# Kernel tuning notes

Hardware: AMD Instinct MI355X
Metric: run time of the kernel (lower is better)

Reference implementation:

```python
import jax, jax.numpy as jnp
import numpy as np

N, E, F, H, L, G = 100000, 1600000, 128, 128, 8, 256
EPS = 1e-5


def setup_inputs() -> dict:
    key = jax.random.key(0)
    ks = jax.random.split(key, 12)
    s = 0.05
    return {
        "x": jax.random.normal(ks[0], (N, F), jnp.float32),
        "edge_index": jax.random.randint(ks[1], (2, E), 0, N, dtype=jnp.int32),
        "batch": jnp.sort(jax.random.randint(ks[2], (N,), 0, G, dtype=jnp.int32)),
        # input projection
        "Wp": jax.random.normal(ks[3], (F, H), jnp.float32) * s,
        "bp": jnp.zeros((H,), jnp.float32),
        # stacked residual-block params (L blocks, 2 GCNConv+BN each)
        "W1": jax.random.normal(ks[4], (L, H, H), jnp.float32) * s,
        "b1": jnp.zeros((L, H), jnp.float32),
        "g1": jnp.ones((L, H), jnp.float32),
        "be1": jnp.zeros((L, H), jnp.float32),
        "W2": jax.random.normal(ks[5], (L, H, H), jnp.float32) * s,
        "b2": jnp.zeros((L, H), jnp.float32),
        "g2": jnp.ones((L, H), jnp.float32),
        "be2": jnp.zeros((L, H), jnp.float32),
        # readout MLP: 3H -> 2H -> H -> 1
        "Wa": jax.random.normal(ks[6], (3 * H, 2 * H), jnp.float32) * s,
        "ba": jnp.zeros((2 * H,), jnp.float32),
        "Wb": jax.random.normal(ks[7], (2 * H, H), jnp.float32) * s,
        "bb": jnp.zeros((H,), jnp.float32),
        "Wc": jax.random.normal(ks[8], (H, 1), jnp.float32) * s,
        "bc": jnp.zeros((1,), jnp.float32),
    }


def _bn(h, g, b):
    # BatchNorm over the node dimension (training-style batch stats, eps=1e-5)
    mu = h.mean(0)
    var = h.var(0)
    return (h - mu) * jax.lax.rsqrt(var + EPS) * g + b


def reference(x, edge_index, batch, Wp, bp, W1, b1, g1, be1, W2, b2, g2, be2,
              Wa, ba, Wb, bb, Wc, bc):
    src, dst = edge_index[0], edge_index[1]
    # GCN symmetric norm with self-loops: deg = in-degree + 1
    deg = jnp.zeros((N,), x.dtype).at[dst].add(1.0) + 1.0
    dinv = jax.lax.rsqrt(deg)
    norm_e = (dinv[src] * dinv[dst])[:, None]   # [E,1]
    self_norm = (dinv * dinv)[:, None]          # [N,1]

    def gcn(h, W, b):
        hw = h @ W                                              # [N,H]
        agg = jnp.zeros_like(hw).at[dst].add(norm_e * hw[src])  # scatter-add over edges
        return agg + self_norm * hw + b                         # self-loop + bias

    h = x @ Wp + bp

    def step(h, p):
        w1, bb1, gg1, bbe1, w2, bb2, gg2, bbe2 = p
        o = jax.nn.relu(_bn(gcn(h, w1, bb1), gg1, bbe1))
        o = _bn(gcn(o, w2, bb2), gg2, bbe2)
        return h + o, None

    h, _ = jax.lax.scan(step, h, (W1, b1, g1, be1, W2, b2, g2, be2))

    sums = jax.ops.segment_sum(h, batch, num_segments=G)
    cnt = jax.ops.segment_sum(jnp.ones((N, 1), h.dtype), batch, num_segments=G)
    mean = sums / jnp.maximum(cnt, 1.0)
    mx = jax.ops.segment_max(h, batch, num_segments=G)
    z = jnp.concatenate([mean, mx, sums], axis=1)  # [G, 3H]

    z = jax.nn.relu(z @ Wa + ba)
    z = jax.nn.relu(z @ Wb + bb)
    return z @ Wc + bc  # [G, 1]
```

## Files before the change

kernel.cpp:

```cpp
#include <hip/hip_runtime.h>
#include <hip/hip_fp16.h>
#include <math.h>
#include <float.h>

#define HDIM 128
#define NGRAPH 256
#define EPSBN 1e-5f
#define PS_REP 32
#define SLABF (2 * PS_REP * 128)

typedef _Float16 f16x8 __attribute__((ext_vector_type(8)));
typedef _Float16 f16x4 __attribute__((ext_vector_type(4)));
typedef float f32x4 __attribute__((ext_vector_type(4)));

__device__ inline unsigned enc_f(float v) {
  unsigned u = __float_as_uint(v);
  return (u & 0x80000000u) ? ~u : (u | 0x80000000u);
}
__device__ inline float dec_f(unsigned e) {
  return __uint_as_float((e & 0x80000000u) ? (e ^ 0x80000000u) : ~e);
}

__global__ void k_deg(const int* __restrict__ dst, int* __restrict__ deg, int E) {
  int i = blockIdx.x * blockDim.x + threadIdx.x;
  if (i < E) atomicAdd(&deg[dst[i]], 1);
}

__global__ void k_dinv(const int* __restrict__ deg, float* __restrict__ dinv, int n) {
  int i = blockIdx.x * blockDim.x + threadIdx.x;
  if (i < n) dinv[i] = rsqrtf((float)deg[i] + 1.0f);
}

__global__ void k_scanA(const int* __restrict__ deg, int* __restrict__ rowstart,
                        int* __restrict__ bsum, int n) {
  __shared__ int s[256];
  int t = threadIdx.x, i = blockIdx.x * 256 + t;
  int v = (i < n) ? ((deg[i] + 3) & ~3) : 0;
  s[t] = v;
  __syncthreads();
  for (int off = 1; off < 256; off <<= 1) {
    int x = (t >= off) ? s[t - off] : 0;
    __syncthreads();
    s[t] += x;
    __syncthreads();
  }
  if (i < n) rowstart[i] = s[t] - v;
  if (t == 255) bsum[blockIdx.x] = s[255];
}

__global__ void k_scanB(int* __restrict__ bsum, int nb) {
  __shared__ int s[512];
  int t = threadIdx.x;
  int v = (t < nb) ? bsum[t] : 0;
  s[t] = v;
  __syncthreads();
  for (int off = 1; off < 512; off <<= 1) {
    int x = (t >= off) ? s[t - off] : 0;
    __syncthreads();
    s[t] += x;
    __syncthreads();
  }
  if (t < nb) bsum[t] = s[t] - v;
}

__global__ void k_scanC(int* __restrict__ rowstart, const int* __restrict__ bsum,
                        const int* __restrict__ deg, int n) {
  int i = blockIdx.x * 256 + threadIdx.x;
  if (i < n) {
    int v = rowstart[i] + bsum[blockIdx.x];
    rowstart[i] = v;
    if (i == n - 1) rowstart[n] = v + ((deg[i] + 3) & ~3);
  }
}

__global__ void k_fill(const int* __restrict__ src, const int* __restrict__ dst,
                       const float* __restrict__ dinv, const int* __restrict__ prow,
                       int* __restrict__ cursor, int2* __restrict__ csr2, int E) {
  int e = blockIdx.x * blockDim.x + threadIdx.x;
  if (e < E) {
    int d = dst[e], s = src[e];
    int pos = prow[d] + atomicAdd(&cursor[d], 1);
    csr2[pos] = make_int2(s << 8, __float_as_int(dinv[s] * dinv[d]));
  }
}

__global__ void k_pad(const int* __restrict__ deg, const int* __restrict__ prow,
                      int2* __restrict__ csr2, int n) {
  int i = blockIdx.x * blockDim.x + threadIdx.x;
  if (i < n) {
    int d = deg[i], dp = (d + 3) & ~3;
    int base = prow[i];
    for (int j = d; j < dp; ++j) csr2[base + j] = make_int2(i << 8, 0);
  }
}

__global__ __launch_bounds__(256) void k_wprep(const float* __restrict__ W1,
                                               const float* __restrict__ W2,
                                               const float* __restrict__ Wp,
                                               _Float16* __restrict__ wt) {
  int m = blockIdx.x;
  const float* Wsrc = (m == 16) ? Wp : (((m & 1) ? W2 : W1) + (size_t)(m >> 1) * 16384);
  _Float16* Wdst = wt + (size_t)m * 16384;
  __shared__ _Float16 lds[128 * 132];
  int t = threadIdx.x;
  const float4* W4 = (const float4*)Wsrc;
  for (int it = 0; it < 16; ++it) {
    int idx = t + it * 256;
    int k = idx >> 5, c4 = idx & 31;
    float4 v = W4[idx];
    lds[(c4 * 4 + 0) * 132 + k] = (_Float16)v.x;
    lds[(c4 * 4 + 1) * 132 + k] = (_Float16)v.y;
    lds[(c4 * 4 + 2) * 132 + k] = (_Float16)v.z;
    lds[(c4 * 4 + 3) * 132 + k] = (_Float16)v.w;
  }
  __syncthreads();
  for (int it = 0; it < 16; ++it) {
    int idx = t + it * 256;
    int col = idx >> 5, k4 = idx & 31;
    f16x4 o;
    o[0] = lds[col * 132 + k4 * 4 + 0];
    o[1] = lds[col * 132 + k4 * 4 + 1];
    o[2] = lds[col * 132 + k4 * 4 + 2];
    o[3] = lds[col * 132 + k4 * 4 + 3];
    *(f16x4*)(Wdst + col * 128 + k4 * 4) = o;
  }
}

__global__ __launch_bounds__(256) void k_gemmp(const float* __restrict__ in,
                                               const _Float16* __restrict__ wt,
                                               const float* __restrict__ bias,
                                               float* __restrict__ out, int n) {
  __shared__ _Float16 As[64 * 128];
  __shared__ _Float16 Bs[128 * 128];
  char* Ap = (char*)As;
  char* Bp = (char*)Bs;
  int tid = threadIdx.x;
  int lane = tid & 63;
  int rt = tid >> 6;
  int row0 = blockIdx.x * 64;

  for (int it = 0; it < 8; ++it) {
    int idx = tid + it * 256;
    int r = idx >> 5, c4 = idx & 31;
    int row = row0 + r;
    if (row >= n) row = n - 1;
    float4 v = *(const float4*)(in + (size_t)row * 128 + c4 * 4);
    f16x4 hv;
    hv[0] = (_Float16)v.x; hv[1] = (_Float16)v.y;
    hv[2] = (_Float16)v.z; hv[3] = (_Float16)v.w;
    *(f16x4*)(Ap + ((r * 256 + c4 * 8) ^ ((r & 7) << 4))) = hv;
  }
  for (int it = 0; it < 8; ++it) {
    int idx = tid + it * 256;
    int col = idx >> 4, k8 = idx & 15;
    f16x8 v = *(const f16x8*)(wt + col * 128 + k8 * 8);
    *(f16x8*)(Bp + ((col * 256 + k8 * 16) ^ ((col & 7) << 4))) = v;
  }
  __syncthreads();

  f32x4 acc[8];
#pragma unroll
  for (int ct = 0; ct < 8; ++ct) acc[ct] = (f32x4){0.f, 0.f, 0.f, 0.f};
  int arow = rt * 16 + (lane & 15);
  int kc = (lane >> 4) * 16;
#pragma unroll
  for (int ks = 0; ks < 4; ++ks) {
    int kb = ks * 64;
    f16x8 a = *(f16x8*)(Ap + ((arow * 256 + kb + kc) ^ ((arow & 7) << 4)));
#pragma unroll
    for (int ct = 0; ct < 8; ++ct) {
      int bcol = ct * 16 + (lane & 15);
      f16x8 b = *(f16x8*)(Bp + ((bcol * 256 + kb + kc) ^ ((bcol & 7) << 4)));
      acc[ct] = __builtin_amdgcn_mfma_f32_16x16x32_f16(a, b, acc[ct], 0, 0, 0);
    }
  }

  int orow0 = row0 + rt * 16 + (lane >> 4) * 4;
#pragma unroll
  for (int ct = 0; ct < 8; ++ct) {
    int col = ct * 16 + (lane & 15);
    float bb = bias[col];
#pragma unroll
    for (int r = 0; r < 4; ++r) {
      int row = orow0 + r;
      if (row < n) out[(size_t)row * 128 + col] = acc[ct][r] + bb;
    }
  }
}

template <int XFORM>
__global__ __launch_bounds__(256) void k_gemmh(const void* __restrict__ inp,
                                               const _Float16* __restrict__ wt,
                                               const float* __restrict__ psumL,
                                               const float* __restrict__ gg,
                                               const float* __restrict__ be,
                                               float* __restrict__ hres,
                                               _Float16* __restrict__ outh, int n) {
  __shared__ _Float16 As[64 * 128];
  __shared__ _Float16 Bs[128 * 128];
  __shared__ float sc_s[128], sh_s[128];
  char* Ap = (char*)As;
  char* Bp = (char*)Bs;
  int tid = threadIdx.x;
  int lane = tid & 63;
  int rt = tid >> 6;
  int row0 = blockIdx.x * 64;

  if (XFORM) {
    if (tid < 128) {
      const float* psqL = psumL + PS_REP * 128;
      float s = 0.f, q = 0.f;
#pragma unroll 8
      for (int r = 0; r < PS_REP; ++r) {
        s += psumL[r * 128 + tid];
        q += psqL[r * 128 + tid];
      }
      float mu = s / (float)n;
      float var = q / (float)n - mu * mu;
      float rs = rsqrtf(var + EPSBN);
      float sc = gg[tid] * rs;
      sc_s[tid] = sc;
      sh_s[tid] = be[tid] - mu * sc;
    }
    __syncthreads();
  }

  if (XFORM == 0) {
    const float* in = (const float*)inp;
    for (int it = 0; it < 8; ++it) {
      int idx = tid + it * 256;
      int r = idx >> 5, c4 = idx & 31;
      int row = row0 + r;
      if (row >= n) row = n - 1;
      float4 v = *(const float4*)(in + (size_t)row * 128 + c4 * 4);
      f16x4 hv16;
      hv16[0] = (_Float16)v.x; hv16[1] = (_Float16)v.y;
      hv16[2] = (_Float16)v.z; hv16[3] = (_Float16)v.w;
      *(f16x4*)(Ap + ((r * 256 + c4 * 8) ^ ((r & 7) << 4))) = hv16;
    }
  } else {
    const _Float16* in = (const _Float16*)inp;
    for (int it = 0; it < 4; ++it) {
      int idx = tid + it * 256;
      int r = idx >> 4, c8 = idx & 15;
      int rrow = row0 + r;
      int row = (rrow >= n) ? (n - 1) : rrow;
      f16x8 tv = *(const f16x8*)(in + (size_t)row * 128 + c8 * 8);
      float4 s0 = *(const float4*)(sc_s + c8 * 8);
      float4 s1 = *(const float4*)(sc_s + c8 * 8 + 4);
      float4 h0 = *(const float4*)(sh_s + c8 * 8);
      float4 h1 = *(const float4*)(sh_s + c8 * 8 + 4);
      float v[8];
#pragma unroll
      for (int j = 0; j < 8; ++j) v[j] = (float)tv[j];
      v[0] = v[0] * s0.x + h0.x; v[1] = v[1] * s0.y + h0.y;
      v[2] = v[2] * s0.z + h0.z; v[3] = v[3] * s0.w + h0.w;
      v[4] = v[4] * s1.x + h1.x; v[5] = v[5] * s1.y + h1.y;
      v[6] = v[6] * s1.z + h1.z; v[7] = v[7] * s1.w + h1.w;
      if (XFORM == 1) {
#pragma unroll
        for (int j = 0; j < 8; ++j) v[j] = fmaxf(v[j], 0.f);
      }
      if (XFORM == 2) {
        float4 hv0 = *(const float4*)(hres + (size_t)row * 128 + c8 * 8);
        float4 hv1 = *(const float4*)(hres + (size_t)row * 128 + c8 * 8 + 4);
        v[0] += hv0.x; v[1] += hv0.y; v[2] += hv0.z; v[3] += hv0.w;
        v[4] += hv1.x; v[5] += hv1.y; v[6] += hv1.z; v[7] += hv1.w;
        if (rrow < n) {
          *(float4*)(hres + (size_t)row * 128 + c8 * 8) = make_float4(v[0], v[1], v[2], v[3]);
          *(float4*)(hres + (size_t)row * 128 + c8 * 8 + 4) = make_float4(v[4], v[5], v[6], v[7]);
        }
      }
      f16x8 o;
#pragma unroll
      for (int j = 0; j < 8; ++j) o[j] = (_Float16)v[j];
      *(f16x8*)(Ap + ((r * 256 + c8 * 16) ^ ((r & 7) << 4))) = o;
    }
  }
  for (int it = 0; it < 8; ++it) {
    int idx = tid + it * 256;
    int col = idx >> 4, k8 = idx & 15;
    f16x8 v = *(const f16x8*)(wt + col * 128 + k8 * 8);
    *(f16x8*)(Bp + ((col * 256 + k8 * 16) ^ ((col & 7) << 4))) = v;
  }
  __syncthreads();

  f32x4 acc[8];
#pragma unroll
  for (int ct = 0; ct < 8; ++ct) acc[ct] = (f32x4){0.f, 0.f, 0.f, 0.f};

  int arow = rt * 16 + (lane & 15);
  int kc = (lane >> 4) * 16;
#pragma unroll
  for (int ks = 0; ks < 4; ++ks) {
    int kb = ks * 64;
    f16x8 a = *(f16x8*)(Ap + ((arow * 256 + kb + kc) ^ ((arow & 7) << 4)));
#pragma unroll
    for (int ct = 0; ct < 8; ++ct) {
      int bcol = ct * 16 + (lane & 15);
      f16x8 b = *(f16x8*)(Bp + ((bcol * 256 + kb + kc) ^ ((bcol & 7) << 4)));
      acc[ct] = __builtin_amdgcn_mfma_f32_16x16x32_f16(a, b, acc[ct], 0, 0, 0);
    }
  }

  int orow0 = row0 + rt * 16 + (lane >> 4) * 4;
#pragma unroll
  for (int ct = 0; ct < 8; ++ct) {
    int col = ct * 16 + (lane & 15);
#pragma unroll
    for (int r = 0; r < 4; ++r) {
      int row = orow0 + r;
      if (row < n) outh[(size_t)row * 128 + col] = (_Float16)acc[ct][r];
    }
  }
}

__global__ __launch_bounds__(256) void k_agg(const _Float16* __restrict__ hw,
                                             const int* __restrict__ prow,
                                             const int2* __restrict__ csr2,
                                             const float* __restrict__ dinv,
                                             const float* __restrict__ bias,
                                             _Float16* __restrict__ out,
                                             float* __restrict__ psumL, int n) {
  int wave = threadIdx.x >> 6;
  int lane = threadIdx.x & 63;
  int grp = lane >> 4;
  int l16 = lane & 15;
  int node = blockIdx.x * 4 + wave;
  float a[8];
#pragma unroll
  for (int j = 0; j < 8; ++j) a[j] = 0.f;

  if (node < n) {
    float b8[8];
#pragma unroll
    for (int j = 0; j < 8; ++j) b8[j] = 0.f;
    int e0 = prow[node], e1 = prow[node + 1];
    int len = e1 - e0;
    int e = e0;
    int end8 = e0 + (len & ~7);
    const char* base = (const char*)hw + l16 * 16;
    for (; e < end8; e += 8) {
      int4 pq = *(const int4*)(csr2 + e + 2 * grp);
      float w0 = __int_as_float(pq.y);
      float w1 = __int_as_float(pq.w);
      f16x8 v0 = *(const f16x8*)(base + (unsigned)pq.x);
      f16x8 v1 = *(const f16x8*)(base + (unsigned)pq.z);
#pragma unroll
      for (int j = 0; j < 8; ++j) {
        a[j] += w0 * (float)v0[j];
        b8[j] += w1 * (float)v1[j];
      }
    }
    if (len & 4) {
      int2 p = csr2[e + grp];
      float w = __int_as_float(p.y);
      f16x8 v = *(const f16x8*)(base + (unsigned)p.x);
#pragma unroll
      for (int j = 0; j < 8; ++j) a[j] += w * (float)v[j];
    }
#pragma unroll
    for (int j = 0; j < 8; ++j) a[j] += b8[j];
#pragma unroll
    for (int j = 0; j < 8; ++j) {
      a[j] += __shfl_xor(a[j], 16);
      a[j] += __shfl_xor(a[j], 32);
    }
    float dn = dinv[node];
    float sn = dn * dn;
    f16x8 v = *(const f16x8*)(hw + (size_t)node * 128 + l16 * 8);
    float4 bb0 = *(const float4*)(bias + l16 * 8);
    float4 bb1 = *(const float4*)(bias + l16 * 8 + 4);
    a[0] += sn * (float)v[0] + bb0.x;
    a[1] += sn * (float)v[1] + bb0.y;
    a[2] += sn * (float)v[2] + bb0.z;
    a[3] += sn * (float)v[3] + bb0.w;
    a[4] += sn * (float)v[4] + bb1.x;
    a[5] += sn * (float)v[5] + bb1.y;
    a[6] += sn * (float)v[6] + bb1.z;
    a[7] += sn * (float)v[7] + bb1.w;
    if (grp == 0) {
      f16x8 ov;
#pragma unroll
      for (int j = 0; j < 8; ++j) ov[j] = (_Float16)a[j];
      *(f16x8*)(out + (size_t)node * 128 + l16 * 8) = ov;
    }
  }
  __shared__ float ss[4][128];
  __shared__ float sq[4][128];
  if (grp == 0) {
    bool live = (node < n);
    float v0 = live ? a[0] : 0.f, v1 = live ? a[1] : 0.f;
    float v2 = live ? a[2] : 0.f, v3 = live ? a[3] : 0.f;
    float v4 = live ? a[4] : 0.f, v5 = live ? a[5] : 0.f;
    float v6 = live ? a[6] : 0.f, v7 = live ? a[7] : 0.f;
    *(float4*)&ss[wave][l16 * 8] = make_float4(v0, v1, v2, v3);
    *(float4*)&ss[wave][l16 * 8 + 4] = make_float4(v4, v5, v6, v7);
    *(float4*)&sq[wave][l16 * 8] = make_float4(v0 * v0, v1 * v1, v2 * v2, v3 * v3);
    *(float4*)&sq[wave][l16 * 8 + 4] = make_float4(v4 * v4, v5 * v5, v6 * v6, v7 * v7);
  }
  __syncthreads();
  int t = threadIdx.x;
  if (t < 128) {
    float s = (ss[0][t] + ss[1][t]) + (ss[2][t] + ss[3][t]);
    float q = (sq[0][t] + sq[1][t]) + (sq[2][t] + sq[3][t]);
    int rep = blockIdx.x & (PS_REP - 1);
    atomicAdd(&psumL[rep * 128 + t], s);
    atomicAdd(&psumL[PS_REP * 128 + rep * 128 + t], q);
  }
}

#define PCHUNK 128
__global__ __launch_bounds__(128) void k_pool(const float* __restrict__ h,
                                              const _Float16* __restrict__ t2h,
                                              const float* __restrict__ psumL,
                                              const float* __restrict__ gg,
                                              const float* __restrict__ be,
                                              const int* __restrict__ batch,
                                              float* __restrict__ sums,
                                              unsigned* __restrict__ maxenc,
                                              int* __restrict__ cnt, int n) {
  int c = threadIdx.x;
  __shared__ float sc_s[128], sh_s[128];
  {
    const float* psqL = psumL + PS_REP * 128;
    float s = 0.f, q = 0.f;
#pragma unroll 8
    for (int r = 0; r < PS_REP; ++r) {
      s += psumL[r * 128 + c];
      q += psqL[r * 128 + c];
    }
    float mu = s / (float)n;
    float var = q / (float)n - mu * mu;
    float rs = rsqrtf(var + EPSBN);
    float sc = gg[c] * rs;
    sc_s[c] = sc;
    sh_s[c] = be[c] - mu * sc;
  }
  __syncthreads();
  float scc = sc_s[c], shc = sh_s[c];

  int start = blockIdx.x * PCHUNK;
  if (start >= n) return;
  int end = start + PCHUNK;
  if (end > n) end = n;
  int cur = batch[start];
  float s = 0.f, mx = -FLT_MAX;
  int runlen = 0;
  for (int i = start; i < end; ++i) {
    int b = batch[i];
    if (b != cur) {
      atomicAdd(&sums[cur * 128 + c], s);
      atomicMax(&maxenc[cur * 128 + c], enc_f(mx));
      if (c == 0) atomicAdd(&cnt[cur], runlen);
      s = 0.f; mx = -FLT_MAX; runlen = 0; cur = b;
    }
    float v = h[(size_t)i * 128 + c] + scc * (float)t2h[(size_t)i * 128 + c] + shc;
    s += v;
    mx = fmaxf(mx, v);
    runlen++;
  }
  atomicAdd(&sums[cur * 128 + c], s);
  atomicMax(&maxenc[cur * 128 + c], enc_f(mx));
  if (c == 0) atomicAdd(&cnt[cur], runlen);
}

__global__ __launch_bounds__(256) void k_readout(const float* __restrict__ sums,
                                                 const unsigned* __restrict__ maxenc,
                                                 const int* __restrict__ cnt,
                                                 const float* __restrict__ Wa,
                                                 const float* __restrict__ ba,
                                                 const float* __restrict__ Wb,
                                                 const float* __restrict__ bb,
                                                 const float* __restrict__ Wc,
                                                 const float* __restrict__ bc,
                                                 float* __restrict__ out) {
  int g = blockIdx.x;
  int t = threadIdx.x;
  __shared__ float z[384];
  __shared__ float za[256];
  __shared__ float zb[128];
  float c = (float)(cnt[g] > 1 ? cnt[g] : 1);
  if (t < 128) {
    float s = sums[g * 128 + t];
    z[t] = s / c;
    z[128 + t] = dec_f(maxenc[g * 128 + t]);
    z[256 + t] = s;
  }
  __syncthreads();
  float accA = ba[t];
  for (int k = 0; k < 384; k++) accA += z[k] * Wa[k * 256 + t];
  za[t] = fmaxf(accA, 0.f);
  __syncthreads();
  if (t < 128) {
    float accB = bb[t];
    for (int k = 0; k < 256; k++) accB += za[k] * Wb[k * 128 + t];
    zb[t] = fmaxf(accB, 0.f);
  }
  __syncthreads();
  if (t < 64) {
    float p = zb[t] * Wc[t] + zb[t + 64] * Wc[t + 64];
    for (int off = 32; off > 0; off >>= 1) p += __shfl_down(p, off);
    if (t == 0) out[g] = p + bc[0];
  }
}

extern "C" void kernel_launch(void* const* d_in, const int* in_sizes, int n_in,
                              void* d_out, int out_size, void* d_ws, size_t ws_size,
                              hipStream_t stream) {
  const float* x   = (const float*)d_in[0];
  const int* edge  = (const int*)d_in[1];
  const int* batch = (const int*)d_in[2];
  const float* Wp  = (const float*)d_in[3];
  const float* bp  = (const float*)d_in[4];
  const float* W1  = (const float*)d_in[5];
  const float* b1  = (const float*)d_in[6];
  const float* g1  = (const float*)d_in[7];
  const float* be1 = (const float*)d_in[8];
  const float* W2  = (const float*)d_in[9];
  const float* b2  = (const float*)d_in[10];
  const float* g2  = (const float*)d_in[11];
  const float* be2 = (const float*)d_in[12];
  const float* Wa  = (const float*)d_in[13];
  const float* ba  = (const float*)d_in[14];
  const float* Wb  = (const float*)d_in[15];
  const float* bbp = (const float*)d_in[16];
  const float* Wc  = (const float*)d_in[17];
  const float* bc  = (const float*)d_in[18];
  float* out = (float*)d_out;

  const int N = in_sizes[0] / 128;
  const int E = in_sizes[1] / 2;
  const int* esrc = edge;
  const int* edst = edge + E;

  char* p = (char*)d_ws;
  auto carve = [&](size_t bytes) {
    char* r = p;
    p += (bytes + 255) & ~(size_t)255;
    return (void*)r;
  };
  float* h    = (float*)carve((size_t)N * 128 * 4);
  _Float16* t1h = (_Float16*)carve((size_t)N * 128 * 2);
  _Float16* t2h = (_Float16*)carve((size_t)N * 128 * 2);
  int2* csr2  = (int2*)carve(((size_t)E + 4 * (size_t)N) * 8);
  int* deg     = (int*)carve((size_t)N * 4);
  float* dinv  = (float*)carve((size_t)N * 4);
  int* prow    = (int*)carve((size_t)(N + 1) * 4);
  int* cursor  = (int*)carve((size_t)N * 4);
  int* bsum    = (int*)carve(512 * 4);
  float* slab  = (float*)carve((size_t)16 * SLABF * 4);
  float* pools = (float*)carve((size_t)NGRAPH * 128 * 4);
  unsigned* poolm = (unsigned*)carve((size_t)NGRAPH * 128 * 4);
  int* poolc      = (int*)carve(NGRAPH * 4);
  _Float16* wt16  = (_Float16*)carve((size_t)17 * 128 * 128 * 2);

  const int NB = (N + 255) / 256;

  hipMemsetAsync(deg, 0, (size_t)N * 4, stream);
  hipMemsetAsync(cursor, 0, (size_t)N * 4, stream);
  hipMemsetAsync(slab, 0, (size_t)16 * SLABF * 4, stream);
  hipMemsetAsync(pools, 0, (size_t)NGRAPH * 128 * 4, stream);
  hipMemsetAsync(poolm, 0, (size_t)NGRAPH * 128 * 4, stream);
  hipMemsetAsync(poolc, 0, (size_t)NGRAPH * 4, stream);

  k_deg<<<(E + 255) / 256, 256, 0, stream>>>(edst, deg, E);
  k_dinv<<<NB, 256, 0, stream>>>(deg, dinv, N);
  k_scanA<<<NB, 256, 0, stream>>>(deg, prow, bsum, N);
  k_scanB<<<1, 512, 0, stream>>>(bsum, NB);
  k_scanC<<<NB, 256, 0, stream>>>(prow, bsum, deg, N);
  k_fill<<<(E + 255) / 256, 256, 0, stream>>>(esrc, edst, dinv, prow, cursor, csr2, E);
  k_pad<<<NB, 256, 0, stream>>>(deg, prow, csr2, N);
  k_wprep<<<17, 256, 0, stream>>>(W1, W2, Wp, wt16);

  const int GB = (N + 63) / 64;
  const int AB = (N + 3) / 4;
  const int PB = (N + PCHUNK - 1) / PCHUNK;

  k_gemmp<<<GB, 256, 0, stream>>>(x, wt16 + (size_t)16 * 16384, bp, h, N);
  k_gemmh<0><<<GB, 256, 0, stream>>>(h, wt16, nullptr, nullptr, nullptr, nullptr, t1h, N);

  for (int l = 0; l < 8; l++) {
    const _Float16* w2t = wt16 + (size_t)(l * 2 + 1) * 16384;
    float* slab1 = slab + (size_t)(2 * l) * SLABF;
    float* slab2 = slab + (size_t)(2 * l + 1) * SLABF;
    k_agg<<<AB, 256, 0, stream>>>(t1h, prow, csr2, dinv, b1 + l * 128, t2h, slab1, N);
    k_gemmh<1><<<GB, 256, 0, stream>>>(t2h, w2t, slab1, g1 + l * 128, be1 + l * 128, nullptr, t1h, N);
    k_agg<<<AB, 256, 0, stream>>>(t1h, prow, csr2, dinv, b2 + l * 128, t2h, slab2, N);
    if (l < 7) {
      const _Float16* w1n = wt16 + (size_t)((l + 1) * 2) * 16384;
      k_gemmh<2><<<GB, 256, 0, stream>>>(t2h, w1n, slab2, g2 + l * 128, be2 + l * 128, h, t1h, N);
    }
  }

  k_pool<<<PB, 128, 0, stream>>>(h, t2h, slab + (size_t)15 * SLABF, g2 + 7 * 128, be2 + 7 * 128,
                                 batch, pools, poolm, poolc, N);
  k_readout<<<NGRAPH, 256, 0, stream>>>(pools, poolm, poolc, Wa, ba, Wb, bbp, Wc, bc, out);
}
```

Measured before the change: 1.732 ms.

## Accumulate aggregation in packed fp16 and split CSR fill into four destination-range passes

```diff
diff --git a/kernel.cpp b/kernel.cpp
--- a/kernel.cpp
+++ b/kernel.cpp
@@ -75,12 +75,16 @@
 
 __global__ void k_fill(const int* __restrict__ src, const int* __restrict__ dst,
                        const float* __restrict__ dinv, const int* __restrict__ prow,
-                       int* __restrict__ cursor, int2* __restrict__ csr2, int E) {
+                       int* __restrict__ cursor, int2* __restrict__ csr2, int E,
+                       int lo, int hi) {
   int e = blockIdx.x * blockDim.x + threadIdx.x;
   if (e < E) {
-    int d = dst[e], s = src[e];
-    int pos = prow[d] + atomicAdd(&cursor[d], 1);
-    csr2[pos] = make_int2(s << 8, __float_as_int(dinv[s] * dinv[d]));
+    int d = dst[e];
+    if (d >= lo && d < hi) {
+      int s = src[e];
+      int pos = prow[d] + atomicAdd(&cursor[d], 1);
+      csr2[pos] = make_int2(s << 8, __float_as_int(dinv[s] * dinv[d]));
+    }
   }
 }
 
@@ -332,9 +336,8 @@
   for (int j = 0; j < 8; ++j) a[j] = 0.f;
 
   if (node < n) {
-    float b8[8];
-#pragma unroll
-    for (int j = 0; j < 8; ++j) b8[j] = 0.f;
+    f16x8 aa = {0, 0, 0, 0, 0, 0, 0, 0};
+    f16x8 ab = {0, 0, 0, 0, 0, 0, 0, 0};
     int e0 = prow[node], e1 = prow[node + 1];
     int len = e1 - e0;
     int e = e0;
@@ -342,25 +345,22 @@
     const char* base = (const char*)hw + l16 * 16;
     for (; e < end8; e += 8) {
       int4 pq = *(const int4*)(csr2 + e + 2 * grp);
-      float w0 = __int_as_float(pq.y);
-      float w1 = __int_as_float(pq.w);
+      _Float16 w0 = (_Float16)__int_as_float(pq.y);
+      _Float16 w1 = (_Float16)__int_as_float(pq.w);
       f16x8 v0 = *(const f16x8*)(base + (unsigned)pq.x);
       f16x8 v1 = *(const f16x8*)(base + (unsigned)pq.z);
-#pragma unroll
-      for (int j = 0; j < 8; ++j) {
-        a[j] += w0 * (float)v0[j];
-        b8[j] += w1 * (float)v1[j];
-      }
+      aa += v0 * w0;
+      ab += v1 * w1;
     }
     if (len & 4) {
       int2 p = csr2[e + grp];
-      float w = __int_as_float(p.y);
+      _Float16 w = (_Float16)__int_as_float(p.y);
       f16x8 v = *(const f16x8*)(base + (unsigned)p.x);
-#pragma unroll
-      for (int j = 0; j < 8; ++j) a[j] += w * (float)v[j];
-    }
-#pragma unroll
-    for (int j = 0; j < 8; ++j) a[j] += b8[j];
+      aa += v * w;
+    }
+    aa += ab;
+#pragma unroll
+    for (int j = 0; j < 8; ++j) a[j] = (float)aa[j];
 #pragma unroll
     for (int j = 0; j < 8; ++j) {
       a[j] += __shfl_xor(a[j], 16);
@@ -569,7 +569,11 @@
   k_scanA<<<NB, 256, 0, stream>>>(deg, prow, bsum, N);
   k_scanB<<<1, 512, 0, stream>>>(bsum, NB);
   k_scanC<<<NB, 256, 0, stream>>>(prow, bsum, deg, N);
-  k_fill<<<(E + 255) / 256, 256, 0, stream>>>(esrc, edst, dinv, prow, cursor, csr2, E);
+  for (int pp = 0; pp < 4; ++pp) {
+    int lo = (int)((long long)N * pp / 4);
+    int hi = (int)((long long)N * (pp + 1) / 4);
+    k_fill<<<(E + 255) / 256, 256, 0, stream>>>(esrc, edst, dinv, prow, cursor, csr2, E, lo, hi);
+  }
   k_pad<<<NB, 256, 0, stream>>>(deg, prow, csr2, N);
   k_wprep<<<17, 256, 0, stream>>>(W1, W2, Wp, wt16);
 
```

Result: slower. 1.776 ms (+2.5%).
